# Kernel tuning notes

Hardware: AMD Instinct MI355X
Metric: run time of the kernel (lower is better)

Reference implementation:

```python
import jax, jax.numpy as jnp
import numpy as np

B, T, D_IN, D_H, D_P = 256, 512, 256, 512, 512

def _lin(k, out_d, in_d):
    # torch nn.Linear default init: U(-1/sqrt(in_d), 1/sqrt(in_d))
    k1, k2 = jax.random.split(k)
    bound = 1.0 / np.sqrt(in_d)
    W = jax.random.uniform(k1, (out_d, in_d), jnp.float32, -bound, bound)
    b = jax.random.uniform(k2, (out_d,), jnp.float32, -bound, bound)
    return W, b

def setup_inputs() -> dict:
    key = jax.random.key(0)
    ks = jax.random.split(key, 8)
    x = jax.random.normal(ks[0], (B, T, D_IN), jnp.float32)
    # RNNCell params (torch init: U(-1/sqrt(hidden), 1/sqrt(hidden)) for all)
    bh = 1.0 / np.sqrt(D_H)
    k = jax.random.split(ks[1], 4)
    W_ih = jax.random.uniform(k[0], (D_H, D_IN), jnp.float32, -bh, bh)
    b_ih = jax.random.uniform(k[1], (D_H,), jnp.float32, -bh, bh)
    W_hh = jax.random.uniform(k[2], (D_H, D_H), jnp.float32, -bh, bh)
    b_hh = jax.random.uniform(k[3], (D_H,), jnp.float32, -bh, bh)
    W_ip, b_ip = _lin(ks[2], D_P, D_IN)
    W_hp, b_hp = _lin(ks[3], D_P, D_H)
    W_g, b_g = _lin(ks[4], D_P, D_IN + D_H)
    W_r, b_r = _lin(ks[5], D_P, D_P)
    W_o, b_o = _lin(ks[6], D_P, D_P)
    return dict(x=x, W_ih=W_ih, b_ih=b_ih, W_hh=W_hh, b_hh=b_hh,
                W_ip=W_ip, b_ip=b_ip, W_hp=W_hp, b_hp=b_hp,
                W_g=W_g, b_g=b_g, W_r=W_r, b_r=b_r, W_o=W_o, b_o=b_o)

def reference(x, W_ih, b_ih, W_hh, b_hh, W_ip, b_ip, W_hp, b_hp,
              W_g, b_g, W_r, b_r, W_o, b_o):
    batch = x.shape[0]
    # Precompute time-parallel projections of x outside the recurrence.
    x_ih = jnp.einsum('bti,hi->bth', x, W_ih) + b_ih + b_hh   # RNN input term
    x_proj_all = jnp.einsum('bti,pi->btp', x, W_ip) + b_ip
    # gate = sigmoid([x_t, h] @ W_g^T + b_g); split W_g into x-part and h-part
    W_gx, W_gh = W_g[:, :x.shape[-1]], W_g[:, x.shape[-1]:]
    gate_x_all = jnp.einsum('bti,pi->btp', x, W_gx) + b_g

    h0 = jnp.zeros((batch, W_hh.shape[0]), x.dtype)

    def step(h, inputs):
        x_ih_t, x_proj, gate_x = inputs
        h = jnp.tanh(x_ih_t + h @ W_hh.T)                # RNNCell (b_ih+b_hh folded in)
        h_proj = h @ W_hp.T + b_hp
        gate = jax.nn.sigmoid(gate_x + h @ W_gh.T)
        blended = gate * h_proj + (1.0 - gate) * x_proj
        res = blended @ W_r.T + b_r
        out_t = jax.nn.relu(res + blended)
        out_t = out_t @ W_o.T + b_o
        return h, out_t

    xs = (jnp.swapaxes(x_ih, 0, 1),       # (T, B, H)
          jnp.swapaxes(x_proj_all, 0, 1), # (T, B, P)
          jnp.swapaxes(gate_x_all, 0, 1)) # (T, B, P)
    _, outs = jax.lax.scan(step, h0, xs)
    return jnp.swapaxes(outs, 0, 1)       # (B, T, P)
```

## Files before the change

kernel.cpp:

```cpp
#include <hip/hip_runtime.h>
#include <hip/hip_bf16.h>
#include <cstdint>

#define RB   256
#define RT   512
#define ROWS (RB*RT)

typedef __attribute__((ext_vector_type(8))) short bf16x8;
typedef __attribute__((ext_vector_type(4))) short s16x4;
typedef __attribute__((ext_vector_type(4))) float f32x4;
typedef unsigned long long ull;

#define DEV static __device__ __forceinline__

DEV float bf2f(unsigned short u){
  union { unsigned int i; float f; } v; v.i = ((unsigned int)u) << 16; return v.f;
}
DEV float blo(unsigned int u){
  union { unsigned int i; float f; } v; v.i = u << 16; return v.f;
}
DEV float bhi(unsigned int u){
  union { unsigned int i; float f; } v; v.i = u & 0xffff0000u; return v.f;
}
DEV unsigned short f2bf(float f){
  union { float f; unsigned int i; } v; v.f = f;
  unsigned int x = v.i;
  return (unsigned short)((x + 0x7fffu + ((x >> 16) & 1u)) >> 16);
}
DEV unsigned int cvt_pk_bf16(float lo, float hi){
  unsigned int r;
  asm("v_cvt_pk_bf16_f32 %0, %1, %2" : "=v"(r) : "v"(lo), "v"(hi));
  return r;
}
DEV float tanh_fast(float x){
  float e  = __expf(2.f * x);
  return 1.f - 2.f * __builtin_amdgcn_rcpf(e + 1.f);
}
DEV float sigmoid_fast(float x){
  float xc = fminf(fmaxf(x, -30.f), 30.f);
  return __builtin_amdgcn_rcpf(1.f + __expf(-xc));
}
DEV void gl_lds16(const void* g, void* l){
  __builtin_amdgcn_global_load_lds(
      (const __attribute__((address_space(1))) unsigned int*)g,
      (__attribute__((address_space(3))) unsigned int*)l, 16, 0, 0);
}

struct ConvArgs {
  const float* src[15];
  unsigned short* dst[15];
  long pre[16];
};

__global__ __launch_bounds__(256) void conv_k(ConvArgs a, long total, ull* gx)
{
  if (blockIdx.x < 512){
    __hip_atomic_store(gx + (size_t)blockIdx.x*256 + threadIdx.x, 0ULL,
                       __ATOMIC_RELAXED, __HIP_MEMORY_SCOPE_SYSTEM);
  }
  long stride = (long)gridDim.x * blockDim.x;
  for (long idx = (long)blockIdx.x * blockDim.x + threadIdx.x; idx < total; idx += stride){
    int t = 0;
    #pragma unroll
    for (int j = 0; j < 14; j++) t += (idx >= a.pre[j + 1]) ? 1 : 0;
    long local = idx - a.pre[t];
    float4 v = ((const float4*)a.src[t])[local];
    s16x4 o;
    o[0] = (short)f2bf(v.x); o[1] = (short)f2bf(v.y);
    o[2] = (short)f2bf(v.z); o[3] = (short)f2bf(v.w);
    ((s16x4*)a.dst[t])[local] = o;
  }
}

__global__ __launch_bounds__(256, 2) void gemm_k(
    const unsigned short* __restrict__ A, int lda,
    const unsigned short* __restrict__ W, int ldb,
    const unsigned short* __restrict__ bias,
    const unsigned short* __restrict__ bias2,
    const unsigned short* __restrict__ addsrc,
    void* __restrict__ C,
    int K, int act, int out_f32)
{
  __shared__ unsigned short As[128*64];
  __shared__ unsigned short Bs[128*64];
  const int tid = threadIdx.x, w = tid >> 6, l = tid & 63;
  const int wm = w >> 1, wn = w & 1;
  const int lr = l & 15, lk = (l >> 4) * 8;
  const long row0 = (long)blockIdx.x * 128;
  const int  col0 = blockIdx.y * 128;

  f32x4 acc[4][4] = {};

  for (int k0 = 0; k0 < K; k0 += 64){
    __syncthreads();
    #pragma unroll
    for (int i = 0; i < 4; i++){
      int chunk = i*256 + tid;
      int r = chunk >> 3, kc = (chunk & 7) * 8;
      gl_lds16(A + (row0 + r)*lda + k0 + kc, (unsigned short*)As + (i*256 + w*64)*8);
      gl_lds16(W + (long)(col0 + r)*ldb + k0 + kc, (unsigned short*)Bs + (i*256 + w*64)*8);
    }
    asm volatile("s_waitcnt vmcnt(0)" ::: "memory");
    __syncthreads();
    #pragma unroll
    for (int ks = 0; ks < 2; ks++){
      bf16x8 a[4], b[4];
      #pragma unroll
      for (int mt = 0; mt < 4; mt++) a[mt] = *(const bf16x8*)&As[(wm*64 + mt*16 + lr)*64 + ks*32 + lk];
      #pragma unroll
      for (int nt = 0; nt < 4; nt++) b[nt] = *(const bf16x8*)&Bs[(wn*64 + nt*16 + lr)*64 + ks*32 + lk];
      #pragma unroll
      for (int mt = 0; mt < 4; mt++)
        #pragma unroll
        for (int nt = 0; nt < 4; nt++)
          acc[mt][nt] = __builtin_amdgcn_mfma_f32_16x16x32_bf16(a[mt], b[nt], acc[mt][nt], 0, 0, 0);
    }
  }

  #pragma unroll
  for (int nt = 0; nt < 4; nt++){
    int c = col0 + wn*64 + nt*16 + lr;
    float bv = bf2f(bias[c]);
    if (bias2) bv += bf2f(bias2[c]);
    #pragma unroll
    for (int mt = 0; mt < 4; mt++){
      #pragma unroll
      for (int i = 0; i < 4; i++){
        long r = row0 + wm*64 + mt*16 + (l >> 4)*4 + i;
        float v = acc[mt][nt][i] + bv;
        if (addsrc) v += bf2f(addsrc[r*512 + c]);
        if (act) v = fmaxf(v, 0.f);
        if (out_f32) ((float*)C)[r*512 + c] = v;
        else ((unsigned short*)C)[r*512 + c] = f2bf(v);
      }
    }
  }
}

__global__ __launch_bounds__(256, 1) void recur_k(
    const unsigned short* __restrict__ xih,
    const unsigned short* __restrict__ Whh,
    unsigned short* __restrict__ H,
    ull* __restrict__ gx)
{
  extern __shared__ unsigned short lds[];
  unsigned short* Wf  = lds;
  unsigned short* hx0 = lds;
  unsigned short* hx1 = lds + 8192;

  const int tid = threadIdx.x, w = tid >> 6, l = tid & 63;
  const int lr = l & 15, hi = l >> 4;
  const int g = blockIdx.x & 15, q = blockIdx.x >> 4;
  const int b0 = g * 16;

  #pragma unroll
  for (int i = 0; i < 32; i++){
    int cid = i*256 + tid;
    int fa = cid >> 6, ln = cid & 63;
    int fw = fa >> 5, fnt = (fa >> 4) & 1, fks = fa & 15;
    int row = q*128 + fw*32 + fnt*16 + (ln & 15);
    int col = fks*32 + (ln >> 4)*8;
    *(bf16x8*)&Wf[cid*8] = *(const bf16x8*)&Whh[row*512 + col];
  }
  __syncthreads();

  bf16x8 wa0[16], wa1[16];
  #pragma unroll
  for (int ks = 0; ks < 16; ks++){
    wa0[ks] = *(const bf16x8*)(Wf + (w*32 +      ks)*512 + l*8);
    wa1[ks] = *(const bf16x8*)(Wf + (w*32 + 16 + ks)*512 + l*8);
  }
  #pragma unroll
  for (int ks = 0; ks < 16; ks++){
    asm volatile("" : "+v"(wa0[ks]));
    asm volatile("" : "+v"(wa1[ks]));
  }
  __syncthreads();

  {
    ull* z = (ull*)lds;
    #pragma unroll
    for (int i = 0; i < 16; i++) z[i*256 + tid] = 0;
  }
  __syncthreads();

  const unsigned short* hrd0 = hx0 + l*8;
  const unsigned short* hrd1 = hx1 + l*8;
  unsigned short*       hwr0 = hx0 + (w*4)*512 + l*8;
  unsigned short*       hwr1 = hx1 + (w*4)*512 + l*8;

  const int colq = q*128 + w*32;
  const long xb = ((long)(b0 + lr) * RT) * 512 + colq + hi*4;
  const unsigned short* xr = xih + xb;
  unsigned short*       hr = H   + xb;

  const int fq = q*4 + w;
  const int e0 = (((hi >> 1)    )*16 + lr)*4 + (hi & 1)*2;
  const int e2 = ((2 + (hi >> 1))*16 + lr)*4 + (hi & 1)*2;

  uint2 xu0 = *(const uint2*)(xr);
  uint2 xu1 = *(const uint2*)(xr + 16);

  for (int t = 0; t < RT; t++){
    const unsigned short* hfb = (t & 1) ? hrd1 : hrd0;
    f32x4 acc0 = {}, acc1 = {};
    #pragma unroll
    for (int ks = 0; ks < 16; ks++){
      bf16x8 hf = *(const bf16x8*)(hfb + ks*512);
      acc0 = __builtin_amdgcn_mfma_f32_16x16x32_bf16(wa0[ks], hf, acc0, 0, 0, 0);
      acc1 = __builtin_amdgcn_mfma_f32_16x16x32_bf16(wa1[ks], hf, acc1, 0, 0, 0);
    }

    uint2 P0, P1;
    {
      float v0 = tanh_fast(acc0[0] + blo(xu0.x));
      float v1 = tanh_fast(acc0[1] + bhi(xu0.x));
      float v2 = tanh_fast(acc0[2] + blo(xu0.y));
      float v3 = tanh_fast(acc0[3] + bhi(xu0.y));
      P0.x = cvt_pk_bf16(v0, v1); P0.y = cvt_pk_bf16(v2, v3);
      float u0 = tanh_fast(acc1[0] + blo(xu1.x));
      float u1 = tanh_fast(acc1[1] + bhi(xu1.x));
      float u2 = tanh_fast(acc1[2] + blo(xu1.y));
      float u3 = tanh_fast(acc1[3] + bhi(xu1.y));
      P1.x = cvt_pk_bf16(u0, u1); P1.y = cvt_pk_bf16(u2, u3);
    }

    {
      const unsigned tghi = (unsigned)(t + 1) << 16;
      ull* gs = gx + ((size_t)((t & 1)*16 + g))*4096 + (size_t)fq*256;
      ull d0 = (ull)(tghi | (P0.x & 0xffffu)) | ((ull)(tghi | (P0.x >> 16)) << 32);
      ull d1 = (ull)(tghi | (P0.y & 0xffffu)) | ((ull)(tghi | (P0.y >> 16)) << 32);
      ull d2 = (ull)(tghi | (P1.x & 0xffffu)) | ((ull)(tghi | (P1.x >> 16)) << 32);
      ull d3 = (ull)(tghi | (P1.y & 0xffffu)) | ((ull)(tghi | (P1.y >> 16)) << 32);
      __hip_atomic_store(gs + e0,     d0, __ATOMIC_RELAXED, __HIP_MEMORY_SCOPE_SYSTEM);
      __hip_atomic_store(gs + e0 + 1, d1, __ATOMIC_RELAXED, __HIP_MEMORY_SCOPE_SYSTEM);
      __hip_atomic_store(gs + e2,     d2, __ATOMIC_RELAXED, __HIP_MEMORY_SCOPE_SYSTEM);
      __hip_atomic_store(gs + e2 + 1, d3, __ATOMIC_RELAXED, __HIP_MEMORY_SCOPE_SYSTEM);
      *(uint2*)(hr)      = P0;
      *(uint2*)(hr + 16) = P1;
      hr += 512;
    }

    if (t + 1 < RT){
      xu0 = *(const uint2*)(xr + 512);
      xu1 = *(const uint2*)(xr + 528);
    }
    xr += 512;

    if (t + 1 < RT){
      const ull* pb = gx + ((size_t)((t & 1)*16 + g))*4096 + (size_t)(w*4)*256 + l*4;
      const unsigned tg = (unsigned)(t + 1);
      ull d[4][4];
      for (;;){
        #pragma unroll
        for (int j = 0; j < 4; j++)
          #pragma unroll
          for (int k = 0; k < 4; k++)
            d[j][k] = __hip_atomic_load(pb + j*256 + k, __ATOMIC_RELAXED, __HIP_MEMORY_SCOPE_SYSTEM);
        unsigned bad = 0;
        #pragma unroll
        for (int j = 0; j < 4; j++)
          #pragma unroll
          for (int k = 0; k < 4; k++)
            bad |= (unsigned)(d[j][k] >> 48) ^ tg;
        if (__all(bad == 0)) break;
      }
      unsigned short* hw = (t & 1) ? hwr0 : hwr1;
      #pragma unroll
      for (int j = 0; j < 4; j++){
        int4 qv;
        qv.x = (int)(((unsigned)(d[j][0] & 0xffffULL)) | ((unsigned)(d[j][0] >> 16) & 0xffff0000u));
        qv.y = (int)(((unsigned)(d[j][1] & 0xffffULL)) | ((unsigned)(d[j][1] >> 16) & 0xffff0000u));
        qv.z = (int)(((unsigned)(d[j][2] & 0xffffULL)) | ((unsigned)(d[j][2] >> 16) & 0xffff0000u));
        qv.w = (int)(((unsigned)(d[j][3] & 0xffffULL)) | ((unsigned)(d[j][3] >> 16) & 0xffff0000u));
        *(int4*)(hw + j*512) = qv;
      }
    }
    __syncthreads();
  }
}

__global__ __launch_bounds__(256, 2) void blend_k(
    const unsigned short* __restrict__ X,
    const unsigned short* __restrict__ Hm,
    const unsigned short* __restrict__ Wg,
    const unsigned short* __restrict__ Wip,
    const unsigned short* __restrict__ Whp,
    const unsigned short* __restrict__ bg,
    const unsigned short* __restrict__ bip,
    const unsigned short* __restrict__ bhp,
    unsigned short* __restrict__ Out)
{
  __shared__ unsigned short As[128*64];
  __shared__ unsigned short Gs[128*64];
  __shared__ unsigned short Ps[128*64];
  const int tid = threadIdx.x, w = tid >> 6, l = tid & 63;
  const int wm = w >> 1, wn = w & 1;
  const int lr = l & 15, lk = (l >> 4) * 8;
  const long row0 = (long)blockIdx.x * 128;
  const int  col0 = blockIdx.y * 128;

  f32x4 accg[4][4] = {}, accp[4][4] = {};
  unsigned int xpp[4][4][2];

  #pragma unroll 1
  for (int k0 = 0; k0 < 768; k0 += 64){
    const bool ph1 = (k0 < 256);
    __syncthreads();
    #pragma unroll
    for (int i = 0; i < 4; i++){
      int chunk = i*256 + tid;
      int r = chunk >> 3, kc = (chunk & 7) * 8;
      const unsigned short* asrc = ph1 ? (X  + (row0 + r)*256 + k0 + kc)
                                       : (Hm + (row0 + r)*512 + (k0 - 256) + kc);
      gl_lds16(asrc, (unsigned short*)As + (i*256 + w*64)*8);
      gl_lds16(Wg + (long)(col0 + r)*768 + k0 + kc, (unsigned short*)Gs + (i*256 + w*64)*8);
      const unsigned short* psrc = ph1 ? (Wip + (col0 + r)*256 + k0 + kc)
                                       : (Whp + (col0 + r)*512 + (k0 - 256) + kc);
      gl_lds16(psrc, (unsigned short*)Ps + (i*256 + w*64)*8);
    }
    asm volatile("s_waitcnt vmcnt(0)" ::: "memory");
    __syncthreads();
    #pragma unroll
    for (int ks = 0; ks < 2; ks++){
      bf16x8 a[4], gq[4], pq[4];
      #pragma unroll
      for (int mt = 0; mt < 4; mt++) a[mt]  = *(const bf16x8*)&As[(wm*64 + mt*16 + lr)*64 + ks*32 + lk];
      #pragma unroll
      for (int nt = 0; nt < 4; nt++){
        gq[nt] = *(const bf16x8*)&Gs[(wn*64 + nt*16 + lr)*64 + ks*32 + lk];
        pq[nt] = *(const bf16x8*)&Ps[(wn*64 + nt*16 + lr)*64 + ks*32 + lk];
      }
      #pragma unroll
      for (int mt = 0; mt < 4; mt++)
        #pragma unroll
        for (int nt = 0; nt < 4; nt++){
          accg[mt][nt] = __builtin_amdgcn_mfma_f32_16x16x32_bf16(a[mt], gq[nt], accg[mt][nt], 0, 0, 0);
          accp[mt][nt] = __builtin_amdgcn_mfma_f32_16x16x32_bf16(a[mt], pq[nt], accp[mt][nt], 0, 0, 0);
        }
    }
    if (k0 == 192){
      #pragma unroll
      for (int mt = 0; mt < 4; mt++)
        #pragma unroll
        for (int nt = 0; nt < 4; nt++){
          xpp[mt][nt][0] = (unsigned)f2bf(accp[mt][nt][0]) | ((unsigned)f2bf(accp[mt][nt][1]) << 16);
          xpp[mt][nt][1] = (unsigned)f2bf(accp[mt][nt][2]) | ((unsigned)f2bf(accp[mt][nt][3]) << 16);
          accp[mt][nt] = (f32x4){0.f, 0.f, 0.f, 0.f};
        }
    }
  }

  #pragma unroll
  for (int nt = 0; nt < 4; nt++){
    int c = col0 + wn*64 + nt*16 + lr;
    float bgv = bf2f(bg[c]), bipv = bf2f(bip[c]), bhpv = bf2f(bhp[c]);
    #pragma unroll
    for (int mt = 0; mt < 4; mt++){
      #pragma unroll
      for (int i = 0; i < 4; i++){
        long r = row0 + wm*64 + mt*16 + (l >> 4)*4 + i;
        float g  = sigmoid_fast(accg[mt][nt][i] + bgv);
        float hp = accp[mt][nt][i] + bhpv;
        unsigned u = xpp[mt][nt][i >> 1];
        float xp = bf2f((unsigned short)((i & 1) ? (u >> 16) : (u & 0xffff))) + bipv;
        float v = g * hp + (1.f - g) * xp;
        Out[r*512 + c] = f2bf(v);
      }
    }
  }
}

extern "C" void kernel_launch(void* const* d_in, const int* in_sizes, int n_in,
                              void* d_out, int out_size, void* d_ws, size_t ws_size,
                              hipStream_t stream)
{
  static const long nelem[15] = {
    (long)ROWS*256,
    512*256, 512,
    512*512, 512,
    512*256, 512,
    512*512, 512,
    512*768, 512,
    512*512, 512,
    512*512, 512
  };

  unsigned char* ob = (unsigned char*)d_out;
  unsigned char* wb = (unsigned char*)d_ws;
  ConvArgs ca;
  long pre = 0;
  size_t doff = 0;
  for (int i = 0; i < 15; i++){
    ca.src[i] = (const float*)d_in[i];
    if (i == 13)      ca.dst[i] = (unsigned short*)(wb + 134217728u);
    else if (i == 14) ca.dst[i] = (unsigned short*)(wb + 134742016u);
    else              ca.dst[i] = (unsigned short*)(ob + doff);
    ca.pre[i] = pre;
    pre += nelem[i] / 4;
    if (i == 0) doff = 67108864u;
    else if (i < 13) doff += (size_t)nelem[i] * 2;
  }
  ca.pre[15] = pre;
  const long total_chunks = pre;

  const unsigned short* xb  = ca.dst[0];
  const unsigned short* Wih = ca.dst[1];
  const unsigned short* bih = ca.dst[2];
  const unsigned short* Whh = ca.dst[3];
  const unsigned short* bhh = ca.dst[4];
  const unsigned short* Wip = ca.dst[5];
  const unsigned short* bip = ca.dst[6];
  const unsigned short* Whp = ca.dst[7];
  const unsigned short* bhp = ca.dst[8];
  const unsigned short* Wg  = ca.dst[9];
  const unsigned short* bg  = ca.dst[10];
  const unsigned short* Wr  = ca.dst[11];
  const unsigned short* br  = ca.dst[12];
  const unsigned short* Wo  = ca.dst[13];
  const unsigned short* bo  = ca.dst[14];

  unsigned short* xih  = (unsigned short*)(ob + 75497472u);
  ull*            gxb  = (ull*)(ob + 209715200u);
  unsigned short* wsb  = (unsigned short*)d_ws;

  dim3 grid(ROWS / 128, 4), block(256);

  conv_k<<<2048, 256, 0, stream>>>(ca, total_chunks, gxb);

  gemm_k<<<grid, block, 0, stream>>>(xb, 256, Wih, 256, bih, bhh, nullptr, xih, 256, 0, 0);

  static const int kRecurLds = 128 * 1024;
  hipFuncSetAttribute((const void*)recur_k, hipFuncAttributeMaxDynamicSharedMemorySize, kRecurLds);
  recur_k<<<64, 256, kRecurLds, stream>>>(xih, Whh, wsb, gxb);

  blend_k<<<grid, block, 0, stream>>>(xb, wsb, Wg, Wip, Whp, bg, bip, bhp, xih);

  gemm_k<<<grid, block, 0, stream>>>(xih, 512, Wr, 512, br, nullptr, xih, wsb, 512, 1, 0);

  gemm_k<<<grid, block, 0, stream>>>(wsb, 512, Wo, 512, bo, nullptr, nullptr, d_out, 512, 0, 1);
}
```

Measured before the change: 2.063 ms.

## Interleave two batch groups per recurrence block to hide cross-block sync latency

Each recurrence block now handles two 16-row batch groups instead of one, and the grid drops from 64 to 32 blocks. The block computes group A's step, publishes it and issues its flag loads, then computes group B while A's exchange is in flight, and only afterwards spins on both. This is meant to hide the global-memory handshake latency between blocks behind the other group's MFMA work. The cost is double the compute per block per step, on half as many CUs.

After: 3.310 ms. +60.4%, slower.

```diff
diff --git a/kernel.cpp b/kernel.cpp
--- a/kernel.cpp
+++ b/kernel.cpp
@@ -144,14 +144,12 @@
     ull* __restrict__ gx)
 {
   extern __shared__ unsigned short lds[];
-  unsigned short* Wf  = lds;
-  unsigned short* hx0 = lds;
-  unsigned short* hx1 = lds + 8192;
+  unsigned short* Wf = lds;
 
   const int tid = threadIdx.x, w = tid >> 6, l = tid & 63;
   const int lr = l & 15, hi = l >> 4;
-  const int g = blockIdx.x & 15, q = blockIdx.x >> 4;
-  const int b0 = g * 16;
+  const int p = blockIdx.x & 7, q = blockIdx.x >> 3;
+  const int gA = p*2, gB = p*2 + 1;
 
   #pragma unroll
   for (int i = 0; i < 32; i++){
@@ -177,57 +175,61 @@
   }
   __syncthreads();
 
+  unsigned short* tA0 = lds;
+  unsigned short* tA1 = lds + 8192;
+  unsigned short* tB0 = lds + 16384;
+  unsigned short* tB1 = lds + 24576;
   {
     ull* z = (ull*)lds;
     #pragma unroll
-    for (int i = 0; i < 16; i++) z[i*256 + tid] = 0;
+    for (int i = 0; i < 32; i++) z[i*256 + tid] = 0;
   }
   __syncthreads();
 
-  const unsigned short* hrd0 = hx0 + l*8;
-  const unsigned short* hrd1 = hx1 + l*8;
-  unsigned short*       hwr0 = hx0 + (w*4)*512 + l*8;
-  unsigned short*       hwr1 = hx1 + (w*4)*512 + l*8;
-
   const int colq = q*128 + w*32;
-  const long xb = ((long)(b0 + lr) * RT) * 512 + colq + hi*4;
-  const unsigned short* xr = xih + xb;
-  unsigned short*       hr = H   + xb;
+  const long xbA = ((long)(gA*16 + lr) * RT) * 512 + colq + hi*4;
+  const long xbB = ((long)(gB*16 + lr) * RT) * 512 + colq + hi*4;
+  const unsigned short* xrA = xih + xbA;
+  const unsigned short* xrB = xih + xbB;
+  unsigned short*       hrA = H   + xbA;
+  unsigned short*       hrB = H   + xbB;
 
   const int fq = q*4 + w;
   const int e0 = (((hi >> 1)    )*16 + lr)*4 + (hi & 1)*2;
   const int e2 = ((2 + (hi >> 1))*16 + lr)*4 + (hi & 1)*2;
 
-  uint2 xu0 = *(const uint2*)(xr);
-  uint2 xu1 = *(const uint2*)(xr + 16);
+  uint2 xuA0 = *(const uint2*)(xrA);
+  uint2 xuA1 = *(const uint2*)(xrA + 16);
+  uint2 xuB0 = *(const uint2*)(xrB);
+  uint2 xuB1 = *(const uint2*)(xrB + 16);
 
   for (int t = 0; t < RT; t++){
-    const unsigned short* hfb = (t & 1) ? hrd1 : hrd0;
-    f32x4 acc0 = {}, acc1 = {};
-    #pragma unroll
-    for (int ks = 0; ks < 16; ks++){
-      bf16x8 hf = *(const bf16x8*)(hfb + ks*512);
-      acc0 = __builtin_amdgcn_mfma_f32_16x16x32_bf16(wa0[ks], hf, acc0, 0, 0, 0);
-      acc1 = __builtin_amdgcn_mfma_f32_16x16x32_bf16(wa1[ks], hf, acc1, 0, 0, 0);
-    }
-
-    uint2 P0, P1;
+    const int par = t & 1;
+    const unsigned tg  = (unsigned)(t + 1);
+    const unsigned tghi = tg << 16;
+
     {
-      float v0 = tanh_fast(acc0[0] + blo(xu0.x));
-      float v1 = tanh_fast(acc0[1] + bhi(xu0.x));
-      float v2 = tanh_fast(acc0[2] + blo(xu0.y));
-      float v3 = tanh_fast(acc0[3] + bhi(xu0.y));
+      const unsigned short* hfb = (par ? tA1 : tA0) + l*8;
+      f32x4 acc0 = {}, acc1 = {};
+      #pragma unroll
+      for (int ks = 0; ks < 16; ks++){
+        bf16x8 hf = *(const bf16x8*)(hfb + ks*512);
+        acc0 = __builtin_amdgcn_mfma_f32_16x16x32_bf16(wa0[ks], hf, acc0, 0, 0, 0);
+        acc1 = __builtin_amdgcn_mfma_f32_16x16x32_bf16(wa1[ks], hf, acc1, 0, 0, 0);
+      }
+      uint2 P0, P1;
+      float v0 = tanh_fast(acc0[0] + blo(xuA0.x));
+      float v1 = tanh_fast(acc0[1] + bhi(xuA0.x));
+      float v2 = tanh_fast(acc0[2] + blo(xuA0.y));
+      float v3 = tanh_fast(acc0[3] + bhi(xuA0.y));
       P0.x = cvt_pk_bf16(v0, v1); P0.y = cvt_pk_bf16(v2, v3);
-      float u0 = tanh_fast(acc1[0] + blo(xu1.x));
-      float u1 = tanh_fast(acc1[1] + bhi(xu1.x));
-      float u2 = tanh_fast(acc1[2] + blo(xu1.y));
-      float u3 = tanh_fast(acc1[3] + bhi(xu1.y));
+      float u0 = tanh_fast(acc1[0] + blo(xuA1.x));
+      float u1 = tanh_fast(acc1[1] + bhi(xuA1.x));
+      float u2 = tanh_fast(acc1[2] + blo(xuA1.y));
+      float u3 = tanh_fast(acc1[3] + bhi(xuA1.y));
       P1.x = cvt_pk_bf16(u0, u1); P1.y = cvt_pk_bf16(u2, u3);
-    }
-
-    {
-      const unsigned tghi = (unsigned)(t + 1) << 16;
-      ull* gs = gx + ((size_t)((t & 1)*16 + g))*4096 + (size_t)fq*256;
+
+      ull* gs = gx + ((size_t)(par*16 + gA))*4096 + (size_t)fq*256;
       ull d0 = (ull)(tghi | (P0.x & 0xffffu)) | ((ull)(tghi | (P0.x >> 16)) << 32);
       ull d1 = (ull)(tghi | (P0.y & 0xffffu)) | ((ull)(tghi | (P0.y >> 16)) << 32);
       ull d2 = (ull)(tghi | (P1.x & 0xffffu)) | ((ull)(tghi | (P1.x >> 16)) << 32);
@@ -236,44 +238,124 @@
       __hip_atomic_store(gs + e0 + 1, d1, __ATOMIC_RELAXED, __HIP_MEMORY_SCOPE_SYSTEM);
       __hip_atomic_store(gs + e2,     d2, __ATOMIC_RELAXED, __HIP_MEMORY_SCOPE_SYSTEM);
       __hip_atomic_store(gs + e2 + 1, d3, __ATOMIC_RELAXED, __HIP_MEMORY_SCOPE_SYSTEM);
-      *(uint2*)(hr)      = P0;
-      *(uint2*)(hr + 16) = P1;
-      hr += 512;
-    }
-
+      *(uint2*)(hrA)      = P0;
+      *(uint2*)(hrA + 16) = P1;
+      hrA += 512;
+    }
     if (t + 1 < RT){
-      xu0 = *(const uint2*)(xr + 512);
-      xu1 = *(const uint2*)(xr + 528);
-    }
-    xr += 512;
-
+      xuA0 = *(const uint2*)(xrA + 512);
+      xuA1 = *(const uint2*)(xrA + 528);
+    }
+    xrA += 512;
+
+    const ull* pbA = gx + ((size_t)(par*16 + gA))*4096 + (size_t)(w*4)*256 + l*4;
+    ull dA[4][4];
+    #pragma unroll
+    for (int j = 0; j < 4; j++)
+      #pragma unroll
+      for (int k = 0; k < 4; k++)
+        dA[j][k] = __hip_atomic_load(pbA + j*256 + k, __ATOMIC_RELAXED, __HIP_MEMORY_SCOPE_SYSTEM);
+
+    {
+      const unsigned short* hfb = (par ? tB1 : tB0) + l*8;
+      f32x4 acc0 = {}, acc1 = {};
+      #pragma unroll
+      for (int ks = 0; ks < 16; ks++){
+        bf16x8 hf = *(const bf16x8*)(hfb + ks*512);
+        acc0 = __builtin_amdgcn_mfma_f32_16x16x32_bf16(wa0[ks], hf, acc0, 0, 0, 0);
+        acc1 = __builtin_amdgcn_mfma_f32_16x16x32_bf16(wa1[ks], hf, acc1, 0, 0, 0);
+      }
+      uint2 P0, P1;
+      float v0 = tanh_fast(acc0[0] + blo(xuB0.x));
+      float v1 = tanh_fast(acc0[1] + bhi(xuB0.x));
+      float v2 = tanh_fast(acc0[2] + blo(xuB0.y));
+      float v3 = tanh_fast(acc0[3] + bhi(xuB0.y));
+      P0.x = cvt_pk_bf16(v0, v1); P0.y = cvt_pk_bf16(v2, v3);
+      float u0 = tanh_fast(acc1[0] + blo(xuB1.x));
+      float u1 = tanh_fast(acc1[1] + bhi(xuB1.x));
+      float u2 = tanh_fast(acc1[2] + blo(xuB1.y));
+      float u3 = tanh_fast(acc1[3] + bhi(xuB1.y));
+      P1.x = cvt_pk_bf16(u0, u1); P1.y = cvt_pk_bf16(u2, u3);
+
+      ull* gs = gx + ((size_t)(par*16 + gB))*4096 + (size_t)fq*256;
+      ull d0 = (ull)(tghi | (P0.x & 0xffffu)) | ((ull)(tghi | (P0.x >> 16)) << 32);
+      ull d1 = (ull)(tghi | (P0.y & 0xffffu)) | ((ull)(tghi | (P0.y >> 16)) << 32);
+      ull d2 = (ull)(tghi | (P1.x & 0xffffu)) | ((ull)(tghi | (P1.x >> 16)) << 32);
+      ull d3 = (ull)(tghi | (P1.y & 0xffffu)) | ((ull)(tghi | (P1.y >> 16)) << 32);
+      __hip_atomic_store(gs + e0,     d0, __ATOMIC_RELAXED, __HIP_MEMORY_SCOPE_SYSTEM);
+      __hip_atomic_store(gs + e0 + 1, d1, __ATOMIC_RELAXED, __HIP_MEMORY_SCOPE_SYSTEM);
+      __hip_atomic_store(gs + e2,     d2, __ATOMIC_RELAXED, __HIP_MEMORY_SCOPE_SYSTEM);
+      __hip_atomic_store(gs + e2 + 1, d3, __ATOMIC_RELAXED, __HIP_MEMORY_SCOPE_SYSTEM);
+      *(uint2*)(hrB)      = P0;
+      *(uint2*)(hrB + 16) = P1;
+      hrB += 512;
+    }
     if (t + 1 < RT){
-      const ull* pb = gx + ((size_t)((t & 1)*16 + g))*4096 + (size_t)(w*4)*256 + l*4;
-      const unsigned tg = (unsigned)(t + 1);
-      ull d[4][4];
+      xuB0 = *(const uint2*)(xrB + 512);
+      xuB1 = *(const uint2*)(xrB + 528);
+    }
+    xrB += 512;
+
+    const ull* pbB = gx + ((size_t)(par*16 + gB))*4096 + (size_t)(w*4)*256 + l*4;
+    ull dB[4][4];
+    #pragma unroll
+    for (int j = 0; j < 4; j++)
+      #pragma unroll
+      for (int k = 0; k < 4; k++)
+        dB[j][k] = __hip_atomic_load(pbB + j*256 + k, __ATOMIC_RELAXED, __HIP_MEMORY_SCOPE_SYSTEM);
+
+    if (t + 1 < RT){
       for (;;){
+        unsigned bad = 0;
         #pragma unroll
         for (int j = 0; j < 4; j++)
           #pragma unroll
           for (int k = 0; k < 4; k++)
-            d[j][k] = __hip_atomic_load(pb + j*256 + k, __ATOMIC_RELAXED, __HIP_MEMORY_SCOPE_SYSTEM);
-        unsigned bad = 0;
+            bad |= (unsigned)(dA[j][k] >> 48) ^ tg;
+        if (__all(bad == 0)) break;
         #pragma unroll
         for (int j = 0; j < 4; j++)
           #pragma unroll
           for (int k = 0; k < 4; k++)
-            bad |= (unsigned)(d[j][k] >> 48) ^ tg;
+            dA[j][k] = __hip_atomic_load(pbA + j*256 + k, __ATOMIC_RELAXED, __HIP_MEMORY_SCOPE_SYSTEM);
+      }
+      {
+        unsigned short* hw = (par ? tA0 : tA1) + (w*4)*512 + l*8;
+        #pragma unroll
+        for (int j = 0; j < 4; j++){
+          int4 qv;
+          qv.x = (int)(((unsigned)(dA[j][0] & 0xffffULL)) | ((unsigned)(dA[j][0] >> 16) & 0xffff0000u));
+          qv.y = (int)(((unsigned)(dA[j][1] & 0xffffULL)) | ((unsigned)(dA[j][1] >> 16) & 0xffff0000u));
+          qv.z = (int)(((unsigned)(dA[j][2] & 0xffffULL)) | ((unsigned)(dA[j][2] >> 16) & 0xffff0000u));
+          qv.w = (int)(((unsigned)(dA[j][3] & 0xffffULL)) | ((unsigned)(dA[j][3] >> 16) & 0xffff0000u));
+          *(int4*)(hw + j*512) = qv;
+        }
+      }
+      for (;;){
+        unsigned bad = 0;
+        #pragma unroll
+        for (int j = 0; j < 4; j++)
+          #pragma unroll
+          for (int k = 0; k < 4; k++)
+            bad |= (unsigned)(dB[j][k] >> 48) ^ tg;
         if (__all(bad == 0)) break;
-      }
-      unsigned short* hw = (t & 1) ? hwr0 : hwr1;
-      #pragma unroll
-      for (int j = 0; j < 4; j++){
-        int4 qv;
-        qv.x = (int)(((unsigned)(d[j][0] & 0xffffULL)) | ((unsigned)(d[j][0] >> 16) & 0xffff0000u));
-        qv.y = (int)(((unsigned)(d[j][1] & 0xffffULL)) | ((unsigned)(d[j][1] >> 16) & 0xffff0000u));
-        qv.z = (int)(((unsigned)(d[j][2] & 0xffffULL)) | ((unsigned)(d[j][2] >> 16) & 0xffff0000u));
-        qv.w = (int)(((unsigned)(d[j][3] & 0xffffULL)) | ((unsigned)(d[j][3] >> 16) & 0xffff0000u));
-        *(int4*)(hw + j*512) = qv;
+        #pragma unroll
+        for (int j = 0; j < 4; j++)
+          #pragma unroll
+          for (int k = 0; k < 4; k++)
+            dB[j][k] = __hip_atomic_load(pbB + j*256 + k, __ATOMIC_RELAXED, __HIP_MEMORY_SCOPE_SYSTEM);
+      }
+      {
+        unsigned short* hw = (par ? tB0 : tB1) + (w*4)*512 + l*8;
+        #pragma unroll
+        for (int j = 0; j < 4; j++){
+          int4 qv;
+          qv.x = (int)(((unsigned)(dB[j][0] & 0xffffULL)) | ((unsigned)(dB[j][0] >> 16) & 0xffff0000u));
+          qv.y = (int)(((unsigned)(dB[j][1] & 0xffffULL)) | ((unsigned)(dB[j][1] >> 16) & 0xffff0000u));
+          qv.z = (int)(((unsigned)(dB[j][2] & 0xffffULL)) | ((unsigned)(dB[j][2] >> 16) & 0xffff0000u));
+          qv.w = (int)(((unsigned)(dB[j][3] & 0xffffULL)) | ((unsigned)(dB[j][3] >> 16) & 0xffff0000u));
+          *(int4*)(hw + j*512) = qv;
+        }
       }
     }
     __syncthreads();
@@ -432,7 +514,7 @@
 
   static const int kRecurLds = 128 * 1024;
   hipFuncSetAttribute((const void*)recur_k, hipFuncAttributeMaxDynamicSharedMemorySize, kRecurLds);
-  recur_k<<<64, 256, kRecurLds, stream>>>(xih, Whh, wsb, gxb);
+  recur_k<<<32, 256, kRecurLds, stream>>>(xih, Whh, wsb, gxb);
 
   blend_k<<<grid, block, 0, stream>>>(xb, wsb, Wg, Wip, Whp, bg, bip, bhp, xih);
 
```

## Double-buffer GEMM loads and vectorize recurrence inter-block exchange with MALL-coherent accesses

Applied to the files above, without the earlier changes.

The GEMM kernel now double-buffers its LDS tiles, issuing the next K-stage's global-to-LDS loads before computing the current one, so load latency overlaps with MFMA work. In the recurrent kernel, the per-step hidden-state exchange between blocks switches from eight-byte atomic stores and loads to 16-byte stores and loads with sc0 sc1 cache bits. The polling loop issues all loads before one wait and adds a short s_sleep before polling. This targets the latency of the serial 512-step cross-block handshake, but relies on inline-asm cache-coherence bits and on 16-byte stores not tearing the tagged payload. The doubled LDS in the GEMM may also reduce occupancy.

After: 2.001 ms. 1.03x faster.

```diff
diff --git a/kernel.cpp b/kernel.cpp
--- a/kernel.cpp
+++ b/kernel.cpp
@@ -9,6 +9,7 @@
 typedef __attribute__((ext_vector_type(8))) short bf16x8;
 typedef __attribute__((ext_vector_type(4))) short s16x4;
 typedef __attribute__((ext_vector_type(4))) float f32x4;
+typedef __attribute__((ext_vector_type(4))) int   i32x4;
 typedef unsigned long long ull;
 
 #define DEV static __device__ __forceinline__
@@ -44,6 +45,16 @@
   __builtin_amdgcn_global_load_lds(
       (const __attribute__((address_space(1))) unsigned int*)g,
       (__attribute__((address_space(3))) unsigned int*)l, 16, 0, 0);
+}
+DEV void st16_mall(void* p, i32x4 v){
+  asm volatile("global_store_dwordx4 %0, %1, off sc0 sc1"
+               :: "v"(p), "v"(v) : "memory");
+}
+DEV i32x4 ld16_mall(const void* p){
+  i32x4 r;
+  asm volatile("global_load_dwordx4 %0, %1, off sc0 sc1"
+               : "=v"(r) : "v"(p) : "memory");
+  return r;
 }
 
 struct ConvArgs {
@@ -81,8 +92,8 @@
     void* __restrict__ C,
     int K, int act, int out_f32)
 {
-  __shared__ unsigned short As[128*64];
-  __shared__ unsigned short Bs[128*64];
+  __shared__ unsigned short As[2][128*64];
+  __shared__ unsigned short Bs[2][128*64];
   const int tid = threadIdx.x, w = tid >> 6, l = tid & 63;
   const int wm = w >> 1, wn = w & 1;
   const int lr = l & 15, lk = (l >> 4) * 8;
@@ -91,31 +102,45 @@
 
   f32x4 acc[4][4] = {};
 
-  for (int k0 = 0; k0 < K; k0 += 64){
-    __syncthreads();
-    #pragma unroll
-    for (int i = 0; i < 4; i++){
-      int chunk = i*256 + tid;
-      int r = chunk >> 3, kc = (chunk & 7) * 8;
-      gl_lds16(A + (row0 + r)*lda + k0 + kc, (unsigned short*)As + (i*256 + w*64)*8);
-      gl_lds16(W + (long)(col0 + r)*ldb + k0 + kc, (unsigned short*)Bs + (i*256 + w*64)*8);
-    }
-    asm volatile("s_waitcnt vmcnt(0)" ::: "memory");
-    __syncthreads();
+#define GSTAGE(buf, kk) { \
+    _Pragma("unroll") \
+    for (int i = 0; i < 4; i++){ \
+      int chunk = i*256 + tid; \
+      int r = chunk >> 3, kc = (chunk & 7) * 8; \
+      gl_lds16(A + (row0 + r)*lda + (kk) + kc, (unsigned short*)As[buf] + (i*256 + w*64)*8); \
+      gl_lds16(W + (long)(col0 + r)*ldb + (kk) + kc, (unsigned short*)Bs[buf] + (i*256 + w*64)*8); \
+    } }
+
+  GSTAGE(0, 0)
+  const int nst = K >> 6;
+  for (int s = 0; s < nst; s++){
+    const int cb = s & 1;
+    if (s + 1 < nst){
+      GSTAGE(cb ^ 1, (s + 1) * 64)
+      asm volatile("s_waitcnt vmcnt(8)" ::: "memory");
+    } else {
+      asm volatile("s_waitcnt vmcnt(0)" ::: "memory");
+    }
+    __builtin_amdgcn_s_barrier();
+    asm volatile("" ::: "memory");
     #pragma unroll
     for (int ks = 0; ks < 2; ks++){
       bf16x8 a[4], b[4];
       #pragma unroll
-      for (int mt = 0; mt < 4; mt++) a[mt] = *(const bf16x8*)&As[(wm*64 + mt*16 + lr)*64 + ks*32 + lk];
-      #pragma unroll
-      for (int nt = 0; nt < 4; nt++) b[nt] = *(const bf16x8*)&Bs[(wn*64 + nt*16 + lr)*64 + ks*32 + lk];
+      for (int mt = 0; mt < 4; mt++) a[mt] = *(const bf16x8*)&As[cb][(wm*64 + mt*16 + lr)*64 + ks*32 + lk];
+      #pragma unroll
+      for (int nt = 0; nt < 4; nt++) b[nt] = *(const bf16x8*)&Bs[cb][(wn*64 + nt*16 + lr)*64 + ks*32 + lk];
       #pragma unroll
       for (int mt = 0; mt < 4; mt++)
         #pragma unroll
         for (int nt = 0; nt < 4; nt++)
           acc[mt][nt] = __builtin_amdgcn_mfma_f32_16x16x32_bf16(a[mt], b[nt], acc[mt][nt], 0, 0, 0);
     }
-  }
+    asm volatile("s_waitcnt lgkmcnt(0)" ::: "memory");
+    __builtin_amdgcn_s_barrier();
+    asm volatile("" ::: "memory");
+  }
+#undef GSTAGE
 
   #pragma unroll
   for (int nt = 0; nt < 4; nt++){
@@ -225,17 +250,17 @@
       P1.x = cvt_pk_bf16(u0, u1); P1.y = cvt_pk_bf16(u2, u3);
     }
 
+    const unsigned tg   = (unsigned)(t + 1);
+    const unsigned tghi = tg << 16;
     {
-      const unsigned tghi = (unsigned)(t + 1) << 16;
       ull* gs = gx + ((size_t)((t & 1)*16 + g))*4096 + (size_t)fq*256;
-      ull d0 = (ull)(tghi | (P0.x & 0xffffu)) | ((ull)(tghi | (P0.x >> 16)) << 32);
-      ull d1 = (ull)(tghi | (P0.y & 0xffffu)) | ((ull)(tghi | (P0.y >> 16)) << 32);
-      ull d2 = (ull)(tghi | (P1.x & 0xffffu)) | ((ull)(tghi | (P1.x >> 16)) << 32);
-      ull d3 = (ull)(tghi | (P1.y & 0xffffu)) | ((ull)(tghi | (P1.y >> 16)) << 32);
-      __hip_atomic_store(gs + e0,     d0, __ATOMIC_RELAXED, __HIP_MEMORY_SCOPE_SYSTEM);
-      __hip_atomic_store(gs + e0 + 1, d1, __ATOMIC_RELAXED, __HIP_MEMORY_SCOPE_SYSTEM);
-      __hip_atomic_store(gs + e2,     d2, __ATOMIC_RELAXED, __HIP_MEMORY_SCOPE_SYSTEM);
-      __hip_atomic_store(gs + e2 + 1, d3, __ATOMIC_RELAXED, __HIP_MEMORY_SCOPE_SYSTEM);
+      i32x4 D0, D1;
+      D0[0] = (int)(tghi | (P0.x & 0xffffu)); D0[1] = (int)(tghi | (P0.x >> 16));
+      D0[2] = (int)(tghi | (P0.y & 0xffffu)); D0[3] = (int)(tghi | (P0.y >> 16));
+      D1[0] = (int)(tghi | (P1.x & 0xffffu)); D1[1] = (int)(tghi | (P1.x >> 16));
+      D1[2] = (int)(tghi | (P1.y & 0xffffu)); D1[3] = (int)(tghi | (P1.y >> 16));
+      st16_mall(gs + e0, D0);
+      st16_mall(gs + e2, D1);
       *(uint2*)(hr)      = P0;
       *(uint2*)(hr + 16) = P1;
       hr += 512;
@@ -248,35 +273,47 @@
     xr += 512;
 
     if (t + 1 < RT){
+      __builtin_amdgcn_s_sleep(7);
       const ull* pb = gx + ((size_t)((t & 1)*16 + g))*4096 + (size_t)(w*4)*256 + l*4;
-      const unsigned tg = (unsigned)(t + 1);
-      ull d[4][4];
+      i32x4 da[8];
+      #pragma unroll
+      for (int j = 0; j < 4; j++){
+        da[2*j]   = ld16_mall(pb + j*256);
+        da[2*j+1] = ld16_mall(pb + j*256 + 2);
+      }
       for (;;){
-        #pragma unroll
-        for (int j = 0; j < 4; j++)
-          #pragma unroll
-          for (int k = 0; k < 4; k++)
-            d[j][k] = __hip_atomic_load(pb + j*256 + k, __ATOMIC_RELAXED, __HIP_MEMORY_SCOPE_SYSTEM);
+        asm volatile("s_waitcnt vmcnt(0)" ::: "memory");
+        __builtin_amdgcn_sched_barrier(0);
         unsigned bad = 0;
         #pragma unroll
-        for (int j = 0; j < 4; j++)
-          #pragma unroll
-          for (int k = 0; k < 4; k++)
-            bad |= (unsigned)(d[j][k] >> 48) ^ tg;
+        for (int j = 0; j < 8; j++){
+          bad |= ((unsigned)da[j][0] >> 16) ^ tg;
+          bad |= ((unsigned)da[j][1] >> 16) ^ tg;
+          bad |= ((unsigned)da[j][2] >> 16) ^ tg;
+          bad |= ((unsigned)da[j][3] >> 16) ^ tg;
+        }
         if (__all(bad == 0)) break;
+        #pragma unroll
+        for (int j = 0; j < 4; j++){
+          da[2*j]   = ld16_mall(pb + j*256);
+          da[2*j+1] = ld16_mall(pb + j*256 + 2);
+        }
       }
       unsigned short* hw = (t & 1) ? hwr0 : hwr1;
       #pragma unroll
       for (int j = 0; j < 4; j++){
-        int4 qv;
-        qv.x = (int)(((unsigned)(d[j][0] & 0xffffULL)) | ((unsigned)(d[j][0] >> 16) & 0xffff0000u));
-        qv.y = (int)(((unsigned)(d[j][1] & 0xffffULL)) | ((unsigned)(d[j][1] >> 16) & 0xffff0000u));
-        qv.z = (int)(((unsigned)(d[j][2] & 0xffffULL)) | ((unsigned)(d[j][2] >> 16) & 0xffff0000u));
-        qv.w = (int)(((unsigned)(d[j][3] & 0xffffULL)) | ((unsigned)(d[j][3] >> 16) & 0xffff0000u));
-        *(int4*)(hw + j*512) = qv;
-      }
-    }
-    __syncthreads();
+        i32x4 a = da[2*j], b = da[2*j+1];
+        i32x4 qv;
+        qv[0] = (a[0] & 0xffff) | (a[1] << 16);
+        qv[1] = (a[2] & 0xffff) | (a[3] << 16);
+        qv[2] = (b[0] & 0xffff) | (b[1] << 16);
+        qv[3] = (b[2] & 0xffff) | (b[3] << 16);
+        *(i32x4*)(hw + j*512) = qv;
+      }
+    }
+    asm volatile("s_waitcnt lgkmcnt(0)" ::: "memory");
+    __builtin_amdgcn_s_barrier();
+    asm volatile("" ::: "memory");
   }
 }
 
@@ -431,7 +468,7 @@
   gemm_k<<<grid, block, 0, stream>>>(xb, 256, Wih, 256, bih, bhh, nullptr, xih, 256, 0, 0);
 
   static const int kRecurLds = 128 * 1024;
-  hipFuncSetAttribute((const void*)recur_k, hipFuncAttributeMaxDynamicSharedMemorySize, kRecurLds);
+  (void)hipFuncSetAttribute((const void*)recur_k, hipFuncAttributeMaxDynamicSharedMemorySize, kRecurLds);
   recur_k<<<64, 256, kRecurLds, stream>>>(xih, Whh, wsb, gxb);
 
   blend_k<<<grid, block, 0, stream>>>(xb, wsb, Wg, Wip, Whp, bg, bip, bhp, xih);
```
